# Kernel optimization log

Measured on AMD Instinct MI355X. Metric: run time of the kernel, lower is better.

## Reference

```python
import jax, jax.numpy as jnp
import numpy as np

B, S, L = 2, 2048, 2048
H, KVH, D = 16, 4, 128
HID = H * D
EPS = 1e-6
SCALE = 1.0 / np.sqrt(D)


def rmsnorm(x, w, eps=EPS):
    # normalize over last dim (head_size), fp32 math
    xf = x.astype(jnp.float32)
    var = jnp.mean(xf * xf, axis=-1, keepdims=True)
    return (xf * jax.lax.rsqrt(var + eps)).astype(x.dtype) * w


def setup_inputs() -> dict:
    key = jax.random.key(0)
    ks = jax.random.split(key, 5)
    s = 1.0 / np.sqrt(HID)
    return {
        "x": jax.random.normal(ks[0], (B, S, HID), jnp.float32),
        "c": jax.random.normal(ks[1], (B, L, HID), jnp.float32),
        "wq": jax.random.normal(ks[2], (HID, H * D), jnp.float32) * s,
        "wkv": jax.random.normal(ks[3], (HID, KVH * D * 2), jnp.float32) * s,
        "wo": jax.random.normal(ks[4], (H * D, HID), jnp.float32) * s,
        "norm_q_w": jnp.ones((D,), jnp.float32),
        "norm_k_w": jnp.ones((D,), jnp.float32),
    }


def reference(x, c, wq, wkv, wo, norm_q_w, norm_k_w):
    bs, seq_len, _ = x.shape
    c_len = c.shape[1]
    n_rep = H // KVH
    # Q projection + per-head RMSNorm
    xq = (x @ wq).reshape(bs, seq_len, H, D)
    xq = rmsnorm(xq, norm_q_w)
    # packed KV projection: view(..., kvh, hd, 2), unbind last dim
    ckv = (c @ wkv).reshape(bs, c_len, KVH, D, 2)
    ck, cv = ckv[..., 0], ckv[..., 1]
    ck = rmsnorm(ck, norm_k_w)
    # GQA repeat_kv (repeat_interleave over head dim)
    ck = jnp.repeat(ck, n_rep, axis=2)  # [b, L, H, D]
    cv = jnp.repeat(cv, n_rep, axis=2)
    # SDPA cross-attention, softmax in fp32
    scores = jnp.einsum("bqhd,bkhd->bhqk", xq, ck) * SCALE
    attn = jax.nn.softmax(scores.astype(jnp.float32), axis=-1).astype(xq.dtype)
    out = jnp.einsum("bhqk,bkhd->bqhd", attn, cv)
    out = out.reshape(bs, seq_len, H * D)
    return out @ wo
```

## Files before the change

kernel.cpp:

```cpp
#include <hip/hip_runtime.h>

#define B_ 2
#define S_ 2048
#define L_ 2048
#define H_ 16
#define KVH_ 4
#define D_ 128
#define HID_ 2048
#define EPS_ 1e-6f

typedef unsigned short u16;
typedef unsigned int u32;
typedef __bf16 bf16x8 __attribute__((ext_vector_type(8)));
typedef float f32x4 __attribute__((ext_vector_type(4)));
typedef unsigned u32x2v __attribute__((ext_vector_type(2)));
typedef unsigned u32x4v __attribute__((ext_vector_type(4)));

__device__ __forceinline__ float bf2f(u32 u) {
  union { u32 i; float f; } x; x.i = u << 16; return x.f;
}
__device__ __forceinline__ u16 f2bf(float f) {
  union { float f; u32 i; } x; x.f = f;
  return (u16)((x.i + 0x7fffu + ((x.i >> 16) & 1u)) >> 16);
}
__device__ __forceinline__ u32 pack_bf16(float a, float b) {
#if __has_builtin(__builtin_amdgcn_cvt_pk_bf16_f32)
  typedef __bf16 bf16x2 __attribute__((ext_vector_type(2)));
  union { bf16x2 v; u32 u; } c;
  c.v = __builtin_amdgcn_cvt_pk_bf16_f32(a, b);
  return c.u;
#else
  return (u32)f2bf(a) | ((u32)f2bf(b) << 16);
#endif
}
__device__ __forceinline__ float fexp2(float x) {
#if __has_builtin(__builtin_amdgcn_exp2f)
  return __builtin_amdgcn_exp2f(x);
#else
  return exp2f(x);
#endif
}
__device__ __forceinline__ void gl2lds16(const u16* g, u16* l) {
  __builtin_amdgcn_global_load_lds(
      (const __attribute__((address_space(1))) u32*)g,
      (__attribute__((address_space(3))) u32*)l, 16, 0, 0);
}

#if __has_builtin(__builtin_amdgcn_permlane32_swap) && __has_builtin(__builtin_amdgcn_permlane16_swap)
#define HAS_PLS 1
#else
#define HAS_PLS 0
#endif

__device__ __forceinline__ u32x4v ctoa(u32 xa, u32 xb, u32 ya, u32 yb,
                                       int quad, int l15) {
  u32x4v f;
#if HAS_PLS
  u32x2v t1 = __builtin_amdgcn_permlane32_swap(xa, ya, false, false);
  u32x2v t2 = __builtin_amdgcn_permlane16_swap(t1.x, t1.y, false, false);
  u32x2v t3 = __builtin_amdgcn_permlane32_swap(xb, yb, false, false);
  u32x2v t4 = __builtin_amdgcn_permlane16_swap(t3.x, t3.y, false, false);
  f.x = t2.x; f.y = t4.x; f.z = t2.y; f.w = t4.y;
#else
  int a0 = (((2 * quad) & 3) * 16 + l15) << 2;
  int a1 = (((2 * quad + 1) & 3) * 16 + l15) << 2;
  u32 xa0 = __builtin_amdgcn_ds_bpermute(a0, xa), ya0 = __builtin_amdgcn_ds_bpermute(a0, ya);
  u32 xb0 = __builtin_amdgcn_ds_bpermute(a0, xb), yb0 = __builtin_amdgcn_ds_bpermute(a0, yb);
  u32 xa1 = __builtin_amdgcn_ds_bpermute(a1, xa), ya1 = __builtin_amdgcn_ds_bpermute(a1, ya);
  u32 xb1 = __builtin_amdgcn_ds_bpermute(a1, xb), yb1 = __builtin_amdgcn_ds_bpermute(a1, yb);
  bool hi = quad >= 2;
  f.x = hi ? ya0 : xa0; f.y = hi ? yb0 : xb0;
  f.z = hi ? ya1 : xa1; f.w = hi ? yb1 : xb1;
#endif
  return f;
}

__global__ __launch_bounds__(256) void cvt_bf16(const float* __restrict__ in,
                                                u16* __restrict__ out, int n4) {
  int i = blockIdx.x * 256 + threadIdx.x;
  if (i >= n4) return;
  float4 v = ((const float4*)in)[i];
  uint2 o;
  o.x = pack_bf16(v.x, v.y);
  o.y = pack_bf16(v.z, v.w);
  ((uint2*)out)[i] = o;
}

__global__ __launch_bounds__(256) void transp_bf16(const float* __restrict__ A,
                                                   u16* __restrict__ At, int R, int C) {
  __shared__ float t[64][65];
  int c0 = blockIdx.x * 64, r0 = blockIdx.y * 64;
  int tx = threadIdx.x & 63, ty = threadIdx.x >> 6;
  for (int i = ty; i < 64; i += 4)
    t[i][tx] = A[(size_t)(r0 + i) * C + c0 + tx];
  __syncthreads();
  for (int i = ty; i < 64; i += 4)
    At[(size_t)(c0 + i) * R + r0 + tx] = f2bf(t[tx][i]);
}

__device__ __forceinline__ void store_out(u16* p, float v) { *p = f2bf(v); }
__device__ __forceinline__ void store_out(float* p, float v) { *p = v; }

template <typename OutT>
__global__ __launch_bounds__(256, 2) void gemm_bt(const u16* __restrict__ A,
                                                  const u16* __restrict__ Bt,
                                                  OutT* __restrict__ C,
                                                  int M, int N, int K) {
  __shared__ u16 sA[128 * 64];
  __shared__ u16 sB[128 * 64];
  const int tid = threadIdx.x;
  const int wave = tid >> 6, lane = tid & 63;
  const int quad = lane >> 4, l15 = lane & 15;
  const int m0 = blockIdx.x * 128, n0 = blockIdx.y * 128;
  const int wm = (wave >> 1) * 64, wn = (wave & 1) * 64;
  const u16* aP = A + (size_t)m0 * K;
  const u16* bP = Bt + (size_t)n0 * K;
  const int sr = lane >> 3;
  const int sc = ((lane & 7) ^ ((lane >> 3) & 7)) * 8;
  const int r0 = wave * 32;
  const int sw = l15 & 7;

  f32x4 acc[4][4];
  for (int i = 0; i < 4; i++)
    for (int j = 0; j < 4; j++)
      for (int r = 0; r < 4; r++) acc[i][j][r] = 0.0f;

  for (int k0 = 0; k0 < K; k0 += 64) {
    for (int is = 0; is < 4; is++) {
      gl2lds16(aP + (size_t)(r0 + is * 8 + sr) * K + k0 + sc, &sA[(r0 + is * 8) * 64]);
      gl2lds16(bP + (size_t)(r0 + is * 8 + sr) * K + k0 + sc, &sB[(r0 + is * 8) * 64]);
    }
    __syncthreads();
    for (int ks = 0; ks < 2; ks++) {
      bf16x8 afrag[4], bfrag[4];
      for (int i = 0; i < 4; i++)
        afrag[i] = *(const bf16x8*)&sA[(wm + i * 16 + l15) * 64 + ((ks * 4 + quad) ^ sw) * 8];
      for (int j = 0; j < 4; j++)
        bfrag[j] = *(const bf16x8*)&sB[(wn + j * 16 + l15) * 64 + ((ks * 4 + quad) ^ sw) * 8];
      for (int i = 0; i < 4; i++)
        for (int j = 0; j < 4; j++)
          acc[i][j] = __builtin_amdgcn_mfma_f32_16x16x32_bf16(afrag[i], bfrag[j], acc[i][j], 0, 0, 0);
    }
    __syncthreads();
  }
  for (int i = 0; i < 4; i++)
    for (int j = 0; j < 4; j++) {
      int row = m0 + wm + i * 16 + quad * 4;
      int col = n0 + wn + j * 16 + l15;
      for (int r = 0; r < 4; r++)
        store_out(&C[(size_t)(row + r) * N + col], acc[i][j][r]);
    }
}

__global__ __launch_bounds__(256) void knorm_deint(const u16* __restrict__ CKV,
                                                   const float* __restrict__ w,
                                                   u16* __restrict__ K,
                                                   u16* __restrict__ Vt) {
  __shared__ u16 vbuf[128][66];
  const int tid = threadIdx.x, wave = tid >> 6, lane = tid & 63;
  const int l0 = blockIdx.x * 64, kvh = blockIdx.y, b = blockIdx.z;
  for (int it = 0; it < 16; it++) {
    int ll = wave * 16 + it;
    int row = b * L_ + l0 + ll;
    const u16* src = CKV + (size_t)row * 1024 + kvh * 256;
    u32 p0 = *(const u32*)&src[lane * 2];
    u32 p1 = *(const u32*)&src[(lane + 64) * 2];
    float k0 = bf2f(p0 & 0xffff), v0 = bf2f(p0 >> 16);
    float k1 = bf2f(p1 & 0xffff), v1 = bf2f(p1 >> 16);
    float ss = k0 * k0 + k1 * k1;
    for (int off = 1; off < 64; off <<= 1) ss += __shfl_xor(ss, off);
    float sc = rsqrtf(ss * (1.0f / 128.0f) + EPS_);
    size_t kb = (((size_t)b * KVH_ + kvh) * L_ + l0 + ll) * D_;
    K[kb + lane] = f2bf(k0 * sc * w[lane]);
    K[kb + lane + 64] = f2bf(k1 * sc * w[lane + 64]);
    vbuf[lane][ll] = f2bf(v0);
    vbuf[lane + 64][ll] = f2bf(v1);
  }
  __syncthreads();
  for (int it = tid; it < 128 * 32; it += 256) {
    int d = it >> 5, cc = (it & 31) * 2;
    u32 pk = (u32)vbuf[d][cc] | ((u32)vbuf[d][cc + 1] << 16);
    *(u32*)&Vt[(((size_t)b * KVH_ + kvh) * D_ + d) * L_ + l0 + cc] = pk;
  }
}

__global__ __launch_bounds__(512, 4) void attn(const u16* __restrict__ XQ,
                                               const float* __restrict__ nw,
                                               const u16* __restrict__ K,
                                               const u16* __restrict__ Vt,
                                               u16* __restrict__ AO) {
  __shared__ u16 sk[2][4][64 * 32];
  __shared__ u16 sv[2][2][128 * 32];
  const int tid = threadIdx.x, wave = tid >> 6, lane = tid & 63;
  const int quad = lane >> 4, l15 = lane & 15;
  const int qt = blockIdx.x, h = blockIdx.y, b = blockIdx.z;
  const int kvh = h >> 2;
  const int s0 = qt * 128, wr0 = wave * 16;

  const u16* kbase = K + ((size_t)(b * KVH_ + kvh) * L_) * D_;
  const u16* vbase = Vt + ((size_t)(b * KVH_ + kvh) * D_) * L_;
  const int srow = lane >> 2;
  const int scol = ((lane & 3) ^ ((lane >> 3) & 3)) * 8;
  const int swq = (quad ^ ((l15 >> 1) & 3)) * 8;
  const int kch = wave >> 1, khalf = wave & 1;
  const int vch = wave >> 2, vqtr = wave & 3;

  auto stage = [&](int l0, int buf) {
    const u16* kb = kbase + (size_t)l0 * D_ + kch * 32;
    for (int is = 0; is < 2; is++) {
      int row = khalf * 32 + is * 16;
      gl2lds16(kb + (size_t)(row + srow) * D_ + scol, &sk[buf][kch][row * 32]);
    }
    const u16* vb = vbase + l0 + vch * 32;
    for (int is = 0; is < 2; is++) {
      int drow = vqtr * 32 + is * 16;
      gl2lds16(vb + (size_t)(drow + srow) * L_ + scol, &sv[buf][vch][drow * 32]);
    }
  };

  bf16x8 qf[4];
  {
    const float cexp = 0.12753102331322172f;
    const u16* qr = XQ + (size_t)(b * S_ + s0 + wr0 + l15) * HID_ + h * D_;
    float vals[4][8];
    float ss = 0.0f;
    for (int kc = 0; kc < 4; kc++) {
      uint4 u = *(const uint4*)&qr[kc * 32 + quad * 8];
      u32 uu[4] = {u.x, u.y, u.z, u.w};
      for (int e = 0; e < 4; e++) {
        float lo = bf2f(uu[e] & 0xffff), hi = bf2f(uu[e] >> 16);
        vals[kc][2 * e] = lo;
        vals[kc][2 * e + 1] = hi;
        ss += lo * lo + hi * hi;
      }
    }
    ss += __shfl_xor(ss, 16);
    ss += __shfl_xor(ss, 32);
    float scale = rsqrtf(ss * (1.0f / 128.0f) + EPS_) * cexp;
    for (int kc = 0; kc < 4; kc++) {
      float4 w0 = *(const float4*)&nw[kc * 32 + quad * 8];
      float4 w1 = *(const float4*)&nw[kc * 32 + quad * 8 + 4];
      union { u32x4v u; bf16x8 v; } q;
      q.u.x = pack_bf16(vals[kc][0] * scale * w0.x, vals[kc][1] * scale * w0.y);
      q.u.y = pack_bf16(vals[kc][2] * scale * w0.z, vals[kc][3] * scale * w0.w);
      q.u.z = pack_bf16(vals[kc][4] * scale * w1.x, vals[kc][5] * scale * w1.y);
      q.u.w = pack_bf16(vals[kc][6] * scale * w1.z, vals[kc][7] * scale * w1.w);
      qf[kc] = q.v;
    }
  }

  float psum = 0.0f;
  f32x4 o[8];
  for (int n = 0; n < 8; n++)
    for (int r = 0; r < 4; r++) o[n][r] = 0.0f;

  stage(0, 0);
  int cur = 0;
  const int NT = L_ / 64;
  for (int t = 0; t < NT; t++) {
    if (t + 1 < NT) {
      stage((t + 1) * 64, cur ^ 1);
      asm volatile("s_waitcnt vmcnt(4)\n\ts_barrier" ::: "memory");
    } else {
      asm volatile("s_waitcnt vmcnt(0)\n\ts_barrier" ::: "memory");
    }

    for (int cc = 0; cc < 2; cc++) {
      f32x4 sacc[2];
      for (int jj = 0; jj < 2; jj++)
        for (int r = 0; r < 4; r++) sacc[jj][r] = 0.0f;
      __builtin_amdgcn_s_setprio(1);
      for (int jj = 0; jj < 2; jj++) {
        int j = cc * 2 + jj;
        for (int kc = 0; kc < 4; kc++) {
          bf16x8 kf = *(const bf16x8*)&sk[cur][kc][(j * 16 + l15) * 32 + swq];
          sacc[jj] = __builtin_amdgcn_mfma_f32_16x16x32_bf16(kf, qf[kc], sacc[jj], 0, 0, 0);
        }
      }
      __builtin_amdgcn_s_setprio(0);
      union { u32x4v u; bf16x8 v; } pf;
      {
        float p0[4], p1[4];
        for (int r = 0; r < 4; r++) {
          p0[r] = fexp2(sacc[0][r]);
          p1[r] = fexp2(sacc[1][r]);
          psum += p0[r] + p1[r];
        }
        u32 xa = pack_bf16(p0[0], p0[1]), xb = pack_bf16(p0[2], p0[3]);
        u32 ya = pack_bf16(p1[0], p1[1]), yb = pack_bf16(p1[2], p1[3]);
        pf.u = ctoa(xa, xb, ya, yb, quad, l15);
      }
      __builtin_amdgcn_s_setprio(1);
      for (int n = 0; n < 8; n++) {
        bf16x8 vf = *(const bf16x8*)&sv[cur][cc][(n * 16 + l15) * 32 + swq];
        o[n] = __builtin_amdgcn_mfma_f32_16x16x32_bf16(pf.v, vf, o[n], 0, 0, 0);
      }
      __builtin_amdgcn_s_setprio(0);
    }
    asm volatile("s_barrier" ::: "memory");
    cur ^= 1;
  }

  {
    float s = psum;
    s += __shfl_xor(s, 16);
    s += __shfl_xor(s, 32);
    float linv = 1.0f / s;
    float lr[4];
    for (int r = 0; r < 4; r++) lr[r] = __shfl(linv, quad * 4 + r);
    u16* ob = AO + (size_t)(b * S_ + s0 + wr0) * HID_ + h * D_;
    for (int n = 0; n < 8; n++)
      for (int r = 0; r < 4; r++)
        ob[(size_t)(quad * 4 + r) * HID_ + n * 16 + l15] = f2bf(o[n][r] * lr[r]);
  }
}

extern "C" void kernel_launch(void* const* d_in, const int* in_sizes, int n_in,
                              void* d_out, int out_size, void* d_ws, size_t ws_size,
                              hipStream_t stream) {
  const float* x = (const float*)d_in[0];
  const float* c = (const float*)d_in[1];
  const float* wq = (const float*)d_in[2];
  const float* wkv = (const float*)d_in[3];
  const float* wo = (const float*)d_in[4];
  const float* nqw = (const float*)d_in[5];
  const float* nkw = (const float*)d_in[6];
  float* out = (float*)d_out;

  const int M = B_ * S_;
  char* p = (char*)d_ws;
  auto alloc = [&](size_t bytes) {
    char* r = p;
    p += (bytes + 255) & ~(size_t)255;
    return r;
  };
  u16* xbf = (u16*)alloc((size_t)M * HID_ * 2);
  u16* cbf = (u16*)alloc((size_t)M * HID_ * 2);
  u16* wqT = (u16*)alloc((size_t)HID_ * HID_ * 2);
  u16* wkvT = (u16*)alloc((size_t)1024 * HID_ * 2);
  u16* woT = (u16*)alloc((size_t)HID_ * HID_ * 2);
  u16* XQ = (u16*)alloc((size_t)M * HID_ * 2);
  u16* CKV = (u16*)alloc((size_t)M * 1024 * 2);
  u16* Kb = (u16*)alloc((size_t)B_ * KVH_ * L_ * D_ * 2);
  u16* Vt = (u16*)alloc((size_t)B_ * KVH_ * D_ * L_ * 2);
  u16* AO = (u16*)alloc((size_t)M * HID_ * 2);

  cvt_bf16<<<8192, 256, 0, stream>>>(x, xbf, M * HID_ / 4);
  cvt_bf16<<<8192, 256, 0, stream>>>(c, cbf, M * HID_ / 4);
  transp_bf16<<<dim3(32, 32), 256, 0, stream>>>(wq, wqT, HID_, HID_);
  transp_bf16<<<dim3(16, 32), 256, 0, stream>>>(wkv, wkvT, HID_, 1024);
  transp_bf16<<<dim3(32, 32), 256, 0, stream>>>(wo, woT, HID_, HID_);
  gemm_bt<u16><<<dim3(32, 16), 256, 0, stream>>>(xbf, wqT, XQ, M, HID_, HID_);
  gemm_bt<u16><<<dim3(32, 8), 256, 0, stream>>>(cbf, wkvT, CKV, M, 1024, HID_);
  knorm_deint<<<dim3(32, 4, 2), 256, 0, stream>>>(CKV, nkw, Kb, Vt);
  attn<<<dim3(16, 16, 2), 512, 0, stream>>>(XQ, nqw, Kb, Vt, AO);
  gemm_bt<float><<<dim3(32, 16), 256, 0, stream>>>(AO, woT, out, M, HID_, HID_);
}
```

Baseline: 361.1 us.

## Double-buffer GEMM LDS loads and merge Q/KV projections and input casts

The GEMM main loop now double-buffers its shared-memory tiles. It issues the next K-tile's global-to-LDS loads before computing on the current tile, and uses explicit vmcnt waits and barriers to overlap the loads with MFMA work. The Q and KV projection GEMMs are merged into one launch that picks its operands by blockIdx.y, and the two fp32-to-bf16 casts become one kernel. This saves launches and tail effects, but doubles LDS use to 64KB per block, which may cut occupancy under launch_bounds(256,2).

```diff
diff --git a/kernel.cpp b/kernel.cpp
--- a/kernel.cpp
+++ b/kernel.cpp
@@ -75,15 +75,21 @@
   return f;
 }
 
-__global__ __launch_bounds__(256) void cvt_bf16(const float* __restrict__ in,
-                                                u16* __restrict__ out, int n4) {
+__global__ __launch_bounds__(256) void cvt2_bf16(const float* __restrict__ a,
+                                                 u16* __restrict__ oa,
+                                                 const float* __restrict__ b,
+                                                 u16* __restrict__ ob, int n4) {
   int i = blockIdx.x * 256 + threadIdx.x;
-  if (i >= n4) return;
-  float4 v = ((const float4*)in)[i];
+  const float* src;
+  u16* dst;
+  int j;
+  if (i < n4) { src = a; dst = oa; j = i; }
+  else { src = b; dst = ob; j = i - n4; }
+  float4 v = ((const float4*)src)[j];
   uint2 o;
   o.x = pack_bf16(v.x, v.y);
   o.y = pack_bf16(v.z, v.w);
-  ((uint2*)out)[i] = o;
+  ((uint2*)dst)[j] = o;
 }
 
 __global__ __launch_bounds__(256) void transp_bf16(const float* __restrict__ A,
@@ -102,46 +108,56 @@
 __device__ __forceinline__ void store_out(float* p, float v) { *p = v; }
 
 template <typename OutT>
-__global__ __launch_bounds__(256, 2) void gemm_bt(const u16* __restrict__ A,
-                                                  const u16* __restrict__ Bt,
-                                                  OutT* __restrict__ C,
-                                                  int M, int N, int K) {
-  __shared__ u16 sA[128 * 64];
-  __shared__ u16 sB[128 * 64];
+__device__ __forceinline__ void gemm_body(const u16* __restrict__ aP,
+                                          const u16* __restrict__ bP,
+                                          OutT* __restrict__ C,
+                                          int m0, int n0, int N, int K,
+                                          u16* sA0, u16* sA1, u16* sB0, u16* sB1) {
   const int tid = threadIdx.x;
   const int wave = tid >> 6, lane = tid & 63;
   const int quad = lane >> 4, l15 = lane & 15;
-  const int m0 = blockIdx.x * 128, n0 = blockIdx.y * 128;
   const int wm = (wave >> 1) * 64, wn = (wave & 1) * 64;
-  const u16* aP = A + (size_t)m0 * K;
-  const u16* bP = Bt + (size_t)n0 * K;
   const int sr = lane >> 3;
   const int sc = ((lane & 7) ^ ((lane >> 3) & 7)) * 8;
   const int r0 = wave * 32;
   const int sw = l15 & 7;
+  u16* sA[2] = {sA0, sA1};
+  u16* sB[2] = {sB0, sB1};
 
   f32x4 acc[4][4];
   for (int i = 0; i < 4; i++)
     for (int j = 0; j < 4; j++)
       for (int r = 0; r < 4; r++) acc[i][j][r] = 0.0f;
 
-  for (int k0 = 0; k0 < K; k0 += 64) {
+  auto stage = [&](int k0, int buf) {
     for (int is = 0; is < 4; is++) {
-      gl2lds16(aP + (size_t)(r0 + is * 8 + sr) * K + k0 + sc, &sA[(r0 + is * 8) * 64]);
-      gl2lds16(bP + (size_t)(r0 + is * 8 + sr) * K + k0 + sc, &sB[(r0 + is * 8) * 64]);
-    }
-    __syncthreads();
+      gl2lds16(aP + (size_t)(r0 + is * 8 + sr) * K + k0 + sc, &sA[buf][(r0 + is * 8) * 64]);
+      gl2lds16(bP + (size_t)(r0 + is * 8 + sr) * K + k0 + sc, &sB[buf][(r0 + is * 8) * 64]);
+    }
+  };
+
+  stage(0, 0);
+  int cur = 0;
+  const int NT = K >> 6;
+  for (int t = 0; t < NT; t++) {
+    if (t + 1 < NT) {
+      stage((t + 1) << 6, cur ^ 1);
+      asm volatile("s_waitcnt vmcnt(8)\n\ts_barrier" ::: "memory");
+    } else {
+      asm volatile("s_waitcnt vmcnt(0)\n\ts_barrier" ::: "memory");
+    }
     for (int ks = 0; ks < 2; ks++) {
       bf16x8 afrag[4], bfrag[4];
       for (int i = 0; i < 4; i++)
-        afrag[i] = *(const bf16x8*)&sA[(wm + i * 16 + l15) * 64 + ((ks * 4 + quad) ^ sw) * 8];
+        afrag[i] = *(const bf16x8*)&sA[cur][(wm + i * 16 + l15) * 64 + ((ks * 4 + quad) ^ sw) * 8];
       for (int j = 0; j < 4; j++)
-        bfrag[j] = *(const bf16x8*)&sB[(wn + j * 16 + l15) * 64 + ((ks * 4 + quad) ^ sw) * 8];
+        bfrag[j] = *(const bf16x8*)&sB[cur][(wn + j * 16 + l15) * 64 + ((ks * 4 + quad) ^ sw) * 8];
       for (int i = 0; i < 4; i++)
         for (int j = 0; j < 4; j++)
           acc[i][j] = __builtin_amdgcn_mfma_f32_16x16x32_bf16(afrag[i], bfrag[j], acc[i][j], 0, 0, 0);
     }
-    __syncthreads();
+    asm volatile("s_barrier" ::: "memory");
+    cur ^= 1;
   }
   for (int i = 0; i < 4; i++)
     for (int j = 0; j < 4; j++) {
@@ -150,6 +166,36 @@
       for (int r = 0; r < 4; r++)
         store_out(&C[(size_t)(row + r) * N + col], acc[i][j][r]);
     }
+}
+
+template <typename OutT>
+__global__ __launch_bounds__(256, 2) void gemm_bt(const u16* __restrict__ A,
+                                                  const u16* __restrict__ Bt,
+                                                  OutT* __restrict__ C,
+                                                  int M, int N, int K) {
+  __shared__ u16 sA[2][128 * 64];
+  __shared__ u16 sB[2][128 * 64];
+  const int m0 = blockIdx.x * 128, n0 = blockIdx.y * 128;
+  gemm_body<OutT>(A + (size_t)m0 * K, Bt + (size_t)n0 * K, C, m0, n0, N, K,
+                  sA[0], sA[1], sB[0], sB[1]);
+}
+
+__global__ __launch_bounds__(256, 2) void gemm_dual(const u16* __restrict__ A1,
+                                                    const u16* __restrict__ B1,
+                                                    u16* __restrict__ C1, int N1,
+                                                    const u16* __restrict__ A2,
+                                                    const u16* __restrict__ B2,
+                                                    u16* __restrict__ C2, int N2,
+                                                    int K, int ny1) {
+  __shared__ u16 sA[2][128 * 64];
+  __shared__ u16 sB[2][128 * 64];
+  const int by = blockIdx.y;
+  const u16* A; const u16* Bt; u16* C; int N, n0;
+  if (by < ny1) { A = A1; Bt = B1; C = C1; N = N1; n0 = by * 128; }
+  else { A = A2; Bt = B2; C = C2; N = N2; n0 = (by - ny1) * 128; }
+  const int m0 = blockIdx.x * 128;
+  gemm_body<u16>(A + (size_t)m0 * K, Bt + (size_t)n0 * K, C, m0, n0, N, K,
+                 sA[0], sA[1], sB[0], sB[1]);
 }
 
 __global__ __launch_bounds__(256) void knorm_deint(const u16* __restrict__ CKV,
@@ -345,13 +391,13 @@
   u16* Vt = (u16*)alloc((size_t)B_ * KVH_ * D_ * L_ * 2);
   u16* AO = (u16*)alloc((size_t)M * HID_ * 2);
 
-  cvt_bf16<<<8192, 256, 0, stream>>>(x, xbf, M * HID_ / 4);
-  cvt_bf16<<<8192, 256, 0, stream>>>(c, cbf, M * HID_ / 4);
+  const int n4 = M * HID_ / 4;
+  cvt2_bf16<<<16384, 256, 0, stream>>>(x, xbf, c, cbf, n4);
   transp_bf16<<<dim3(32, 32), 256, 0, stream>>>(wq, wqT, HID_, HID_);
   transp_bf16<<<dim3(16, 32), 256, 0, stream>>>(wkv, wkvT, HID_, 1024);
   transp_bf16<<<dim3(32, 32), 256, 0, stream>>>(wo, woT, HID_, HID_);
-  gemm_bt<u16><<<dim3(32, 16), 256, 0, stream>>>(xbf, wqT, XQ, M, HID_, HID_);
-  gemm_bt<u16><<<dim3(32, 8), 256, 0, stream>>>(cbf, wkvT, CKV, M, 1024, HID_);
+  gemm_dual<<<dim3(32, 24), 256, 0, stream>>>(xbf, wqT, XQ, HID_,
+                                              cbf, wkvT, CKV, 1024, HID_, 16);
   knorm_deint<<<dim3(32, 4, 2), 256, 0, stream>>>(CKV, nkw, Kb, Vt);
   attn<<<dim3(16, 16, 2), 512, 0, stream>>>(XQ, nqw, Kb, Vt, AO);
   gemm_bt<float><<<dim3(32, 16), 256, 0, stream>>>(AO, woT, out, M, HID_, HID_);
```

Result: slower. 387.6 us (+7.3%).
